# Performance work log

Measured on AMD Instinct MI355X. Metric: run time of the kernel, lower is better.

## Reference

```python
import jax, jax.numpy as jnp
import numpy as np

WINDOW = 7
N_HEADS = 4
EMBED = 128
N_TOK = WINDOW * WINDOW  # 49
N_WIN = 64               # windows per image (56x56 feature map / 7)
BATCH_IMG = 64
B = N_WIN * BATCH_IMG    # 4096


def make_rel_index(w):
    ch = np.arange(w)
    coords = np.stack(np.meshgrid(ch, ch), axis=0).reshape(2, -1)  # (2, w*w)
    rel = coords[:, :, None] - coords[:, None, :]                  # (2, N, N)
    rel = rel.transpose(1, 2, 0)
    rel[:, :, 0] += w - 1
    rel[:, :, 1] += w - 1
    rel[:, :, 0] *= 2 * w - 1
    return jnp.asarray(rel.sum(-1), dtype=jnp.int32)               # (N, N)


def setup_inputs() -> dict:
    key = jax.random.key(0)
    ks = jax.random.split(key, 6)
    x = jax.random.normal(ks[0], (B, N_TOK, EMBED), dtype=jnp.float32)
    qkv_w = jax.random.normal(ks[1], (EMBED, 3 * EMBED), dtype=jnp.float32) * (EMBED ** -0.5)
    qkv_b = jnp.zeros((3 * EMBED,), dtype=jnp.float32)
    proj_w = jax.random.normal(ks[2], (EMBED, EMBED), dtype=jnp.float32) * (EMBED ** -0.5)
    proj_b = jnp.zeros((EMBED,), dtype=jnp.float32)
    bias_table = jax.random.normal(ks[3], ((2 * WINDOW - 1) ** 2, N_HEADS), dtype=jnp.float32) * 0.02
    # shift mask: additive, 0 or large negative; use random binary * -100 to mimic Swin shift mask
    mask_bits = jax.random.bernoulli(ks[4], 0.2, (N_WIN, N_TOK, N_TOK))
    mask = jnp.where(mask_bits, jnp.float32(-100.0), jnp.float32(0.0))
    rel_index = make_rel_index(WINDOW)
    return {"x": x, "qkv_w": qkv_w, "qkv_b": qkv_b, "proj_w": proj_w,
            "proj_b": proj_b, "bias_table": bias_table, "mask": mask,
            "rel_index": rel_index}


def reference(x, qkv_w, qkv_b, proj_w, proj_b, bias_table, mask, rel_index):
    Bt, N, C = x.shape
    h = N_HEADS
    d = C // h
    scale = d ** -0.5
    qkv = (x @ qkv_w + qkv_b).reshape(Bt, N, 3, h, d)
    q, k, v = jnp.moveaxis(qkv, 2, 0)                      # each (B, N, h, d)
    q = q * scale
    attn = jnp.einsum('bnhd,bmhd->bhnm', q, k)             # (B, h, N, N)
    bias = bias_table[rel_index.reshape(-1)].reshape(N, N, h)
    attn = attn + jnp.transpose(bias, (2, 0, 1))[None]     # add rel-pos bias
    nW = mask.shape[0]
    attn = attn.reshape(Bt // nW, nW, h, N, N) + mask[None, :, None]
    attn = jax.nn.softmax(attn.reshape(Bt, h, N, N), axis=-1)
    out = jnp.einsum('bhnm,bmhd->bnhd', attn, v).reshape(Bt, N, C)
    return out @ proj_w + proj_b
```

## Files before the change

kernel.cpp:

```cpp
#include <hip/hip_runtime.h>

#define NTOK 49
#define CDIM 128
#define NH 4
#define NWIN 64

typedef unsigned short u16;
typedef unsigned int u32;
typedef __bf16 bf16x8 __attribute__((ext_vector_type(8)));
typedef float f32x4 __attribute__((ext_vector_type(4)));
typedef u16 u16x4 __attribute__((ext_vector_type(4)));

__device__ __forceinline__ u16 f2bf(float f) {
  u32 u = __float_as_uint(f);
  u += 0x7fffu + ((u >> 16) & 1u);
  return (u16)(u >> 16);
}
__device__ __forceinline__ u32 pack2(float a, float b) {
  return (u32)f2bf(a) | ((u32)f2bf(b) << 16);
}
__device__ __forceinline__ bf16x8 ld8(const u16* p) { return *(const bf16x8*)p; }

#define DPP_ADD(v, ctrl)                                                            \
  v += __int_as_float(__builtin_amdgcn_update_dpp(0, __float_as_int(v), ctrl, 0xf, 0xf, true))

__global__ void prep_kernel(const float* __restrict__ qkv_w,
                            const float* __restrict__ proj_w,
                            const float* __restrict__ bias_table,
                            const float* __restrict__ mask,
                            const int* __restrict__ rel_index,
                            u16* __restrict__ wqkvT,
                            u16* __restrict__ wprojT,
                            float* __restrict__ cmbT) {
  int i = blockIdx.x * 256 + threadIdx.x;
  if (i < 384 * 128) {
    int n = i >> 7, k = i & 127;
    wqkvT[i] = f2bf(qkv_w[k * 384 + n]);
  }
  if (i < 128 * 128) {
    int n = i >> 7, k = i & 127;
    wprojT[i] = f2bf(proj_w[k * 128 + n]);
  }
  int n = i & 63, m = (i >> 6) & 63, hh = (i >> 12) & 3, win = i >> 14;
  float v = -1e30f;
  if (n < NTOK && m < NTOK)
    v = bias_table[rel_index[n * NTOK + m] * NH + hh] + mask[(win * NTOK + n) * NTOK + m];
  cmbT[i] = v;
}

#define RGN(h) (8192 + (h) * 4608)

__device__ __forceinline__ int xsw(int row, int col) {
  return (row << 7) + ((((col >> 3) ^ (row & 15)) << 3) | (col & 7));
}

__global__ __launch_bounds__(256, 3)
void swin_fused(const float* __restrict__ x, const float* __restrict__ qkv_b,
                const float* __restrict__ proj_b, const u16* __restrict__ wqkvT,
                const u16* __restrict__ wprojT, const float* __restrict__ cmbT,
                float* __restrict__ out) {
  __shared__ u16 lds[26624];
  const int tid  = threadIdx.x;
  const int w    = tid >> 6;
  const int lane = tid & 63;
  const int ln   = lane & 15;
  const int quad = lane >> 4;
  const int b    = blockIdx.x;
  const int win  = b & (NWIN - 1);
  const float scale = 0.17677669529663687f;

  {
    const float4* x4 = (const float4*)(x + (size_t)b * (NTOK * CDIM));
    for (int i = tid; i < (NTOK * CDIM) / 4; i += 256) {
      float4 f = x4[i];
      int e = i << 2;
      int row = e >> 7, col = e & 127;
      u16x4 v;
      v[0] = f2bf(f.x); v[1] = f2bf(f.y); v[2] = f2bf(f.z); v[3] = f2bf(f.w);
      *(u16x4*)&lds[xsw(row, col)] = v;
    }
    for (int i = tid; i < (15 * CDIM) / 4; i += 256) {
      int e = i << 2;
      int row = NTOK + (e >> 7), col = e & 127;
      u16x4 v = {0, 0, 0, 0};
      *(u16x4*)&lds[xsw(row, col)] = v;
    }
  }
  __syncthreads();

  u32 vbx[4][2], vby[4][2];
  {
    bf16x8 af[4][4];
#pragma unroll
    for (int tm = 0; tm < 4; ++tm)
#pragma unroll
      for (int ks = 0; ks < 4; ++ks)
        af[tm][ks] = ld8(&lds[xsw(tm * 16 + ln, ks * 32 + quad * 8)]);

#pragma unroll
    for (int tl = 0; tl < 6; ++tl) {
      int sect = tl >> 1, tc = tl & 1;
      int colg = sect * 128 + w * 32 + tc * 16 + ln;
      bf16x8 bw[4];
#pragma unroll
      for (int ks = 0; ks < 4; ++ks)
        bw[ks] = ld8(wqkvT + colg * 128 + ks * 32 + quad * 8);
      float cb = qkv_b[colg];
#pragma unroll
      for (int tm = 0; tm < 4; ++tm) {
        f32x4 acc = {0.f, 0.f, 0.f, 0.f};
#pragma unroll
        for (int ks = 0; ks < 4; ++ks)
          acc = __builtin_amdgcn_mfma_f32_16x16x32_bf16(af[tm][ks], bw[ks], acc, 0, 0, 0);
        int row0 = tm * 16 + quad * 4;
        if (sect == 0) {
#pragma unroll
          for (int r = 0; r < 4; ++r)
            lds[RGN(w) + (row0 + r) * 36 + tc * 16 + ln] = f2bf((acc[r] + cb) * scale);
        } else if (sect == 1) {
#pragma unroll
          for (int r = 0; r < 4; ++r)
            lds[RGN(w) + 2304 + (row0 + r) * 36 + tc * 16 + ln] = f2bf(acc[r] + cb);
        } else {
          vbx[tm][tc] = pack2(acc[0] + cb, acc[1] + cb);
          vby[tm][tc] = pack2(acc[2] + cb, acc[3] + cb);
        }
      }
    }
  }

  f32x4 s[4][4];
  {
    bf16x8 aq[4];
#pragma unroll
    for (int tm = 0; tm < 4; ++tm)
      aq[tm] = ld8(&lds[RGN(w) + (tm * 16 + ln) * 36 + quad * 8]);
#pragma unroll
    for (int tn = 0; tn < 4; ++tn) {
      bf16x8 bk = ld8(&lds[RGN(w) + 2304 + (tn * 16 + ln) * 36 + quad * 8]);
#pragma unroll
      for (int tm = 0; tm < 4; ++tm) {
        f32x4 z = {0.f, 0.f, 0.f, 0.f};
        s[tm][tn] = __builtin_amdgcn_mfma_f32_16x16x32_bf16(aq[tm], bk, z, 0, 0, 0);
      }
    }
  }
  {
    const float* cb = cmbT + ((size_t)((win << 2) | w) << 12);
#pragma unroll
    for (int tm = 0; tm < 4; ++tm) {
#pragma unroll
      for (int tn = 0; tn < 4; ++tn) {
        f32x4 c4 = *(const f32x4*)&cb[(tn * 16 + ln) * 64 + tm * 16 + quad * 4];
        s[tm][tn] += c4;
      }
    }
  }
  float inv[4][4];
#pragma unroll
  for (int tm = 0; tm < 4; ++tm) {
    int row0 = tm * 16 + quad * 4;
#pragma unroll
    for (int r = 0; r < 4; ++r) {
      float e0 = __expf(s[tm][0][r]);
      float e1 = __expf(s[tm][1][r]);
      float e2 = __expf(s[tm][2][r]);
      float e3 = __expf(s[tm][3][r]);
      float t = (e0 + e1) + (e2 + e3);
      DPP_ADD(t, 0xB1);
      DPP_ADD(t, 0x4E);
      DPP_ADD(t, 0x124);
      DPP_ADD(t, 0x128);
      inv[tm][r] = 1.0f / t;
      int rr = row0 + r;
      lds[RGN(w) + rr * 68 + 0 * 16 + ln] = f2bf(e0);
      lds[RGN(w) + rr * 68 + 1 * 16 + ln] = f2bf(e1);
      lds[RGN(w) + rr * 68 + 2 * 16 + ln] = f2bf(e2);
      lds[RGN(w) + rr * 68 + 3 * 16 + ln] = f2bf(e3);
    }
  }

  {
    f32x4 o[4][2];
#pragma unroll
    for (int tm = 0; tm < 4; ++tm)
#pragma unroll
      for (int tc = 0; tc < 2; ++tc) { f32x4 z = {0.f,0.f,0.f,0.f}; o[tm][tc] = z; }
#pragma unroll
    for (int ks = 0; ks < 2; ++ks) {
      bf16x8 pa[4];
#pragma unroll
      for (int tm = 0; tm < 4; ++tm)
        pa[tm] = ld8(&lds[RGN(w) + (tm * 16 + ln) * 68 + ks * 32 + quad * 8]);
#pragma unroll
      for (int tc = 0; tc < 2; ++tc) {
        union { u32 u[4]; bf16x8 v; } bv;
#pragma unroll
        for (int p = 0; p < 4; ++p) {
          int src = ((2 * (quad & 1) + (p >> 1)) << 4) | ln;
          int a0 = __shfl((int)((p & 1) ? vby[2 * ks][tc]     : vbx[2 * ks][tc]),     src);
          int a1 = __shfl((int)((p & 1) ? vby[2 * ks + 1][tc] : vbx[2 * ks + 1][tc]), src);
          bv.u[p] = (u32)((quad < 2) ? a0 : a1);
        }
#pragma unroll
        for (int tm = 0; tm < 4; ++tm)
          o[tm][tc] = __builtin_amdgcn_mfma_f32_16x16x32_bf16(pa[tm], bv.v, o[tm][tc], 0, 0, 0);
      }
    }
#pragma unroll
    for (int tm = 0; tm < 4; ++tm) {
      int row0 = tm * 16 + quad * 4;
#pragma unroll
      for (int tc = 0; tc < 2; ++tc)
#pragma unroll
        for (int r = 0; r < 4; ++r)
          lds[RGN(w) + 2304 + (row0 + r) * 36 + tc * 16 + ln] = f2bf(o[tm][tc][r] * inv[tm][r]);
    }
  }
  __syncthreads();

  {
    bf16x8 aof[4][4];
#pragma unroll
    for (int tm = 0; tm < 4; ++tm)
#pragma unroll
      for (int ks = 0; ks < 4; ++ks)
        aof[tm][ks] = ld8(&lds[RGN(ks) + 2304 + (tm * 16 + ln) * 36 + quad * 8]);
#pragma unroll
    for (int tj = 0; tj < 2; ++tj) {
      int colg = w * 32 + tj * 16 + ln;
      bf16x8 bw[4];
#pragma unroll
      for (int ks = 0; ks < 4; ++ks)
        bw[ks] = ld8(wprojT + colg * 128 + ks * 32 + quad * 8);
      float pb = proj_b[colg];
#pragma unroll
      for (int tm = 0; tm < 4; ++tm) {
        f32x4 acc = {0.f, 0.f, 0.f, 0.f};
#pragma unroll
        for (int ks = 0; ks < 4; ++ks)
          acc = __builtin_amdgcn_mfma_f32_16x16x32_bf16(aof[tm][ks], bw[ks], acc, 0, 0, 0);
        int row0 = tm * 16 + quad * 4;
#pragma unroll
        for (int r = 0; r < 4; ++r) {
          int rr = row0 + r;
          if (rr < NTOK)
            out[((size_t)b * NTOK + rr) * CDIM + colg] = acc[r] + pb;
        }
      }
    }
  }
}

extern "C" void kernel_launch(void* const* d_in, const int* in_sizes, int n_in,
                              void* d_out, int out_size, void* d_ws, size_t ws_size,
                              hipStream_t stream) {
  const float* x          = (const float*)d_in[0];
  const float* qkv_w      = (const float*)d_in[1];
  const float* qkv_b      = (const float*)d_in[2];
  const float* proj_w     = (const float*)d_in[3];
  const float* proj_b     = (const float*)d_in[4];
  const float* bias_table = (const float*)d_in[5];
  const float* mask       = (const float*)d_in[6];
  const int*   rel_index  = (const int*)d_in[7];

  u16*   wqkvT  = (u16*)d_ws;
  u16*   wprojT = wqkvT + 384 * 128;
  float* cmbT   = (float*)((char*)d_ws + 131072);

  const int Bt = in_sizes[0] / (NTOK * CDIM);

  prep_kernel<<<4096, 256, 0, stream>>>(qkv_w, proj_w, bias_table, mask, rel_index,
                                        wqkvT, wprojT, cmbT);
  swin_fused<<<Bt, 256, 0, stream>>>(x, qkv_b, proj_b, wqkvT, wprojT, cmbT, (float*)d_out);
}
```

Before: 303.0 us.

## Load x directly into MFMA registers, drop LDS staging, split prep kernels

```diff
diff --git a/kernel.cpp b/kernel.cpp
--- a/kernel.cpp
+++ b/kernel.cpp
@@ -16,50 +16,69 @@
   u += 0x7fffu + ((u >> 16) & 1u);
   return (u16)(u >> 16);
 }
-__device__ __forceinline__ u32 pack2(float a, float b) {
-  return (u32)f2bf(a) | ((u32)f2bf(b) << 16);
+__device__ __forceinline__ u32 cvtpk(float a, float b) {
+  u32 r;
+  asm("v_cvt_pk_bf16_f32 %0, %1, %2" : "=v"(r) : "v"(a), "v"(b));
+  return r;
+}
+__device__ __forceinline__ bf16x8 pk8(float4 a, float4 b) {
+  union { u32 u[4]; bf16x8 v; } r;
+  r.u[0] = cvtpk(a.x, a.y); r.u[1] = cvtpk(a.z, a.w);
+  r.u[2] = cvtpk(b.x, b.y); r.u[3] = cvtpk(b.z, b.w);
+  return r.v;
 }
 __device__ __forceinline__ bf16x8 ld8(const u16* p) { return *(const bf16x8*)p; }
 
 #define DPP_ADD(v, ctrl)                                                            \
   v += __int_as_float(__builtin_amdgcn_update_dpp(0, __float_as_int(v), ctrl, 0xf, 0xf, true))
 
-__global__ void prep_kernel(const float* __restrict__ qkv_w,
-                            const float* __restrict__ proj_w,
-                            const float* __restrict__ bias_table,
-                            const float* __restrict__ mask,
-                            const int* __restrict__ rel_index,
-                            u16* __restrict__ wqkvT,
-                            u16* __restrict__ wprojT,
-                            float* __restrict__ cmbT) {
+__global__ void prep_w(const float* __restrict__ qkv_w, const float* __restrict__ proj_w,
+                       u16* __restrict__ wqkvT, u16* __restrict__ wprojT) {
   int i = blockIdx.x * 256 + threadIdx.x;
   if (i < 384 * 128) {
     int n = i >> 7, k = i & 127;
     wqkvT[i] = f2bf(qkv_w[k * 384 + n]);
-  }
-  if (i < 128 * 128) {
-    int n = i >> 7, k = i & 127;
-    wprojT[i] = f2bf(proj_w[k * 128 + n]);
-  }
-  int n = i & 63, m = (i >> 6) & 63, hh = (i >> 12) & 3, win = i >> 14;
-  float v = -1e30f;
-  if (n < NTOK && m < NTOK)
-    v = bias_table[rel_index[n * NTOK + m] * NH + hh] + mask[(win * NTOK + n) * NTOK + m];
-  cmbT[i] = v;
-}
-
-#define RGN(h) (8192 + (h) * 4608)
-
-__device__ __forceinline__ int xsw(int row, int col) {
-  return (row << 7) + ((((col >> 3) ^ (row & 15)) << 3) | (col & 7));
-}
-
-__global__ __launch_bounds__(256, 3)
+  } else {
+    int j = i - 384 * 128;
+    int n = j >> 7, k = j & 127;
+    wprojT[j] = f2bf(proj_w[k * 128 + n]);
+  }
+}
+
+__global__ void prep_cmb(const float* __restrict__ bias_table,
+                         const float* __restrict__ mask,
+                         const int* __restrict__ rel_index,
+                         float* __restrict__ cmbT) {
+  const int win = blockIdx.x >> 2, h = blockIdx.x & 3;
+  __shared__ float t[64 * 65];
+  const int m0 = threadIdx.x & 63;
+  const int n0 = threadIdx.x >> 6;
+#pragma unroll
+  for (int it = 0; it < 16; ++it) {
+    int n = it * 4 + n0;
+    float v = -1e30f;
+    if (n < NTOK && m0 < NTOK)
+      v = bias_table[rel_index[n * NTOK + m0] * NH + h] + mask[(win * NTOK + n) * NTOK + m0];
+    t[m0 * 65 + n] = v;
+  }
+  __syncthreads();
+  const int n1 = threadIdx.x & 63, m1 = threadIdx.x >> 6;
+  float* dst = cmbT + ((size_t)blockIdx.x << 12);
+#pragma unroll
+  for (int it = 0; it < 16; ++it) {
+    int m = it * 4 + m1;
+    dst[m * 64 + n1] = t[m * 65 + n1];
+  }
+}
+
+#define RGN(h) ((h) * 4608)
+
+__global__ __launch_bounds__(256, 4)
 void swin_fused(const float* __restrict__ x, const float* __restrict__ qkv_b,
                 const float* __restrict__ proj_b, const u16* __restrict__ wqkvT,
                 const u16* __restrict__ wprojT, const float* __restrict__ cmbT,
-                float* __restrict__ out) {
-  __shared__ u16 lds[26624];
+                float* __restrict__ out, int total_tok) {
+  __shared__ u16 lds[18432];
   const int tid  = threadIdx.x;
   const int w    = tid >> 6;
   const int lane = tid & 63;
@@ -69,62 +88,48 @@
   const int win  = b & (NWIN - 1);
   const float scale = 0.17677669529663687f;
 
-  {
-    const float4* x4 = (const float4*)(x + (size_t)b * (NTOK * CDIM));
-    for (int i = tid; i < (NTOK * CDIM) / 4; i += 256) {
-      float4 f = x4[i];
-      int e = i << 2;
-      int row = e >> 7, col = e & 127;
-      u16x4 v;
-      v[0] = f2bf(f.x); v[1] = f2bf(f.y); v[2] = f2bf(f.z); v[3] = f2bf(f.w);
-      *(u16x4*)&lds[xsw(row, col)] = v;
-    }
-    for (int i = tid; i < (15 * CDIM) / 4; i += 256) {
-      int e = i << 2;
-      int row = NTOK + (e >> 7), col = e & 127;
-      u16x4 v = {0, 0, 0, 0};
-      *(u16x4*)&lds[xsw(row, col)] = v;
-    }
-  }
-  __syncthreads();
+  bf16x8 af[4][4];
+#pragma unroll
+  for (int tm = 0; tm < 4; ++tm) {
+    long gtok = (long)b * NTOK + tm * 16 + ln;
+    if (gtok >= total_tok) gtok = total_tok - 1;
+    const float* rp = x + gtok * CDIM + quad * 8;
+#pragma unroll
+    for (int ks = 0; ks < 4; ++ks) {
+      float4 f0 = *(const float4*)(rp + ks * 32);
+      float4 f1 = *(const float4*)(rp + ks * 32 + 4);
+      af[tm][ks] = pk8(f0, f1);
+    }
+  }
 
   u32 vbx[4][2], vby[4][2];
-  {
-    bf16x8 af[4][4];
-#pragma unroll
-    for (int tm = 0; tm < 4; ++tm)
+#pragma unroll
+  for (int tl = 0; tl < 6; ++tl) {
+    int sect = tl >> 1, tc = tl & 1;
+    int colg = sect * 128 + w * 32 + tc * 16 + ln;
+    bf16x8 bw[4];
+#pragma unroll
+    for (int ks = 0; ks < 4; ++ks)
+      bw[ks] = ld8(wqkvT + colg * 128 + ks * 32 + quad * 8);
+    float cb = qkv_b[colg];
+#pragma unroll
+    for (int tm = 0; tm < 4; ++tm) {
+      f32x4 acc = {0.f, 0.f, 0.f, 0.f};
 #pragma unroll
       for (int ks = 0; ks < 4; ++ks)
-        af[tm][ks] = ld8(&lds[xsw(tm * 16 + ln, ks * 32 + quad * 8)]);
-
-#pragma unroll
-    for (int tl = 0; tl < 6; ++tl) {
-      int sect = tl >> 1, tc = tl & 1;
-      int colg = sect * 128 + w * 32 + tc * 16 + ln;
-      bf16x8 bw[4];
-#pragma unroll
-      for (int ks = 0; ks < 4; ++ks)
-        bw[ks] = ld8(wqkvT + colg * 128 + ks * 32 + quad * 8);
-      float cb = qkv_b[colg];
-#pragma unroll
-      for (int tm = 0; tm < 4; ++tm) {
-        f32x4 acc = {0.f, 0.f, 0.f, 0.f};
-#pragma unroll
-        for (int ks = 0; ks < 4; ++ks)
-          acc = __builtin_amdgcn_mfma_f32_16x16x32_bf16(af[tm][ks], bw[ks], acc, 0, 0, 0);
-        int row0 = tm * 16 + quad * 4;
-        if (sect == 0) {
-#pragma unroll
-          for (int r = 0; r < 4; ++r)
-            lds[RGN(w) + (row0 + r) * 36 + tc * 16 + ln] = f2bf((acc[r] + cb) * scale);
-        } else if (sect == 1) {
-#pragma unroll
-          for (int r = 0; r < 4; ++r)
-            lds[RGN(w) + 2304 + (row0 + r) * 36 + tc * 16 + ln] = f2bf(acc[r] + cb);
-        } else {
-          vbx[tm][tc] = pack2(acc[0] + cb, acc[1] + cb);
-          vby[tm][tc] = pack2(acc[2] + cb, acc[3] + cb);
-        }
+        acc = __builtin_amdgcn_mfma_f32_16x16x32_bf16(af[tm][ks], bw[ks], acc, 0, 0, 0);
+      int row0 = tm * 16 + quad * 4;
+      if (sect == 0) {
+#pragma unroll
+        for (int r = 0; r < 4; ++r)
+          lds[RGN(w) + (row0 + r) * 36 + tc * 16 + ln] = f2bf((acc[r] + cb) * scale);
+      } else if (sect == 1) {
+#pragma unroll
+        for (int r = 0; r < 4; ++r)
+          lds[RGN(w) + 2304 + (row0 + r) * 36 + tc * 16 + ln] = f2bf(acc[r] + cb);
+      } else {
+        vbx[tm][tc] = cvtpk(acc[0] + cb, acc[1] + cb);
+        vby[tm][tc] = cvtpk(acc[2] + cb, acc[3] + cb);
       }
     }
   }
@@ -148,13 +153,12 @@
   {
     const float* cb = cmbT + ((size_t)((win << 2) | w) << 12);
 #pragma unroll
-    for (int tm = 0; tm < 4; ++tm) {
+    for (int tm = 0; tm < 4; ++tm)
 #pragma unroll
       for (int tn = 0; tn < 4; ++tn) {
         f32x4 c4 = *(const f32x4*)&cb[(tn * 16 + ln) * 64 + tm * 16 + quad * 4];
         s[tm][tn] += c4;
       }
-    }
   }
   float inv[4][4];
 #pragma unroll
@@ -173,10 +177,12 @@
       DPP_ADD(t, 0x128);
       inv[tm][r] = 1.0f / t;
       int rr = row0 + r;
-      lds[RGN(w) + rr * 68 + 0 * 16 + ln] = f2bf(e0);
-      lds[RGN(w) + rr * 68 + 1 * 16 + ln] = f2bf(e1);
-      lds[RGN(w) + rr * 68 + 2 * 16 + ln] = f2bf(e2);
-      lds[RGN(w) + rr * 68 + 3 * 16 + ln] = f2bf(e3);
+      u32 p01 = cvtpk(e0, e1);
+      u32 p23 = cvtpk(e2, e3);
+      lds[RGN(w) + rr * 68 + 0 * 16 + ln] = (u16)p01;
+      lds[RGN(w) + rr * 68 + 1 * 16 + ln] = (u16)(p01 >> 16);
+      lds[RGN(w) + rr * 68 + 2 * 16 + ln] = (u16)p23;
+      lds[RGN(w) + rr * 68 + 3 * 16 + ln] = (u16)(p23 >> 16);
     }
   }
 
@@ -211,10 +217,11 @@
     for (int tm = 0; tm < 4; ++tm) {
       int row0 = tm * 16 + quad * 4;
 #pragma unroll
-      for (int tc = 0; tc < 2; ++tc)
-#pragma unroll
-        for (int r = 0; r < 4; ++r)
-          lds[RGN(w) + 2304 + (row0 + r) * 36 + tc * 16 + ln] = f2bf(o[tm][tc][r] * inv[tm][r]);
+      for (int r = 0; r < 4; ++r) {
+        u32 pq = cvtpk(o[tm][0][r] * inv[tm][r], o[tm][1][r] * inv[tm][r]);
+        lds[RGN(w) + 2304 + (row0 + r) * 36 + 0 * 16 + ln] = (u16)pq;
+        lds[RGN(w) + 2304 + (row0 + r) * 36 + 1 * 16 + ln] = (u16)(pq >> 16);
+      }
     }
   }
   __syncthreads();
@@ -270,7 +277,8 @@
 
   const int Bt = in_sizes[0] / (NTOK * CDIM);
 
-  prep_kernel<<<4096, 256, 0, stream>>>(qkv_w, proj_w, bias_table, mask, rel_index,
-                                        wqkvT, wprojT, cmbT);
-  swin_fused<<<Bt, 256, 0, stream>>>(x, qkv_b, proj_b, wqkvT, wprojT, cmbT, (float*)d_out);
-}
+  prep_w<<<256, 256, 0, stream>>>(qkv_w, proj_w, wqkvT, wprojT);
+  prep_cmb<<<256, 256, 0, stream>>>(bias_table, mask, rel_index, cmbT);
+  swin_fused<<<Bt, 256, 0, stream>>>(x, qkv_b, proj_b, wqkvT, wprojT, cmbT,
+                                     (float*)d_out, Bt * NTOK);
+}
```

New measurement: 343.2 us. 1.13x slower.
